# Performance work log

Hardware: AMD Instinct MI355X
Metric: run time of the kernel (lower is better)

Reference implementation:

```python
import jax, jax.numpy as jnp
import numpy as np

N = 50000
E = 800000
D = 64

def setup_inputs() -> dict:
    key = jax.random.key(0)
    k1, k2, k3, k4 = jax.random.split(key, 4)
    node_features = jax.random.normal(k1, (N, D), dtype=jnp.float32)
    edge_index = jax.random.randint(k2, (E, 2), 0, N, dtype=jnp.int64)
    W = jax.random.normal(k3, (D, D), dtype=jnp.float32) * (1.0 / np.sqrt(D))
    b_lin = jax.random.normal(k4, (D,), dtype=jnp.float32) * 0.02
    bias = jnp.zeros((D,), dtype=jnp.float32)
    return {"node_features": node_features, "edge_index": edge_index,
            "W": W, "b_lin": b_lin, "bias": bias}

def reference(node_features, edge_index, W, b_lin, bias):
    # linear: [N, D_in] @ [D_in, D_out]
    x = node_features @ W.T + b_lin
    src = edge_index[:, 0]
    dst = edge_index[:, 1]
    n = x.shape[0]
    # scatter-add of gathered source features into destination nodes
    aggregated = jax.ops.segment_sum(x[src], dst, num_segments=n)
    degree = jax.ops.segment_sum(jnp.ones((src.shape[0],), x.dtype), dst,
                                 num_segments=n)
    degree = jnp.maximum(degree, 1.0)
    x = x + aggregated / degree[:, None]
    return jax.nn.relu(x + bias)
```

## Files before the change

kernel.cpp:

```cpp
#include <hip/hip_runtime.h>
#include <hip/hip_bf16.h>

#define NN 50000
#define DD 64
#define EE 800000
#define NB 196
#define NTILE 3125
#define NSLICE 128
#define ESL 6250
#define DRNG 6250
#define BCAP 64

typedef unsigned short u16;
typedef unsigned int u32;
typedef __attribute__((ext_vector_type(8))) short bf16x8;
typedef __attribute__((ext_vector_type(4))) float f32x4;

__device__ __forceinline__ float bf2f(u16 u) {
  u32 t = ((u32)u) << 16;
  return __builtin_bit_cast(float, t);
}
__device__ __forceinline__ u16 f2bf(float f) {
  u32 b = __builtin_bit_cast(u32, f);
  u32 r = (b + 0x7FFF + ((b >> 16) & 1)) >> 16;
  return (u16)r;
}

__global__ __launch_bounds__(256) void linear_mfma_kernel(
    const float* __restrict__ nf, const float* __restrict__ W,
    const float* __restrict__ b_lin, u16* __restrict__ x16,
    int* __restrict__ cnt) {
  __shared__ u16 Wsh[64 * 72];
  int tid = threadIdx.x;

  if (blockIdx.x < NB) {
    int zi = blockIdx.x * 256 + tid;
    if (zi < NN) cnt[zi] = 0;
  }

#pragma unroll
  for (int s = 0; s < 16; ++s) {
    int idx = s * 256 + tid;
    int j = idx >> 6, k = idx & 63;
    Wsh[j * 72 + k] = f2bf(W[idx]);
  }
  __syncthreads();

  int wave = tid >> 6;
  int lane = tid & 63;
  int tile = blockIdx.x * 4 + wave;
  if (tile >= NTILE) return;

  int m = lane & 15;
  int quad = lane >> 4;
  int rowbase = tile * 16;

  bf16x8 bfrag[4][2];
#pragma unroll
  for (int c = 0; c < 4; ++c) {
#pragma unroll
    for (int ks = 0; ks < 2; ++ks) {
      const u16* p = &Wsh[(c * 16 + m) * 72 + ks * 32 + quad * 8];
      bfrag[c][ks] = *(const bf16x8*)p;
    }
  }

  bf16x8 afrag[2];
#pragma unroll
  for (int ks = 0; ks < 2; ++ks) {
    const float* p = nf + (rowbase + m) * DD + ks * 32 + quad * 8;
    float4 lo = *(const float4*)p;
    float4 hi = *(const float4*)(p + 4);
    bf16x8 a;
    a[0] = (short)f2bf(lo.x); a[1] = (short)f2bf(lo.y);
    a[2] = (short)f2bf(lo.z); a[3] = (short)f2bf(lo.w);
    a[4] = (short)f2bf(hi.x); a[5] = (short)f2bf(hi.y);
    a[6] = (short)f2bf(hi.z); a[7] = (short)f2bf(hi.w);
    afrag[ks] = a;
  }

  f32x4 acc[4];
#pragma unroll
  for (int c = 0; c < 4; ++c) {
    acc[c][0] = 0.0f; acc[c][1] = 0.0f; acc[c][2] = 0.0f; acc[c][3] = 0.0f;
  }
#pragma unroll
  for (int c = 0; c < 4; ++c) {
    acc[c] = __builtin_amdgcn_mfma_f32_16x16x32_bf16(afrag[0], bfrag[c][0], acc[c], 0, 0, 0);
    acc[c] = __builtin_amdgcn_mfma_f32_16x16x32_bf16(afrag[1], bfrag[c][1], acc[c], 0, 0, 0);
  }

#pragma unroll
  for (int c = 0; c < 4; ++c) {
    int gcol = c * 16 + m;
    float bl = b_lin[gcol];
#pragma unroll
    for (int r = 0; r < 4; ++r) {
      int grow = rowbase + quad * 4 + r;
      x16[grow * DD + gcol] = f2bf(acc[c][r] + bl);
    }
  }
}

__global__ __launch_bounds__(256) void scatter_kernel(
    const int* __restrict__ ei, int* __restrict__ cnt,
    u16* __restrict__ bucket) {
  int r = blockIdx.x & 7;
  int sl = blockIdx.x >> 3;
  int rlo = r * DRNG;
  int ebase = sl * ESL;
  int eend = ebase + ESL;
#pragma unroll 1
  for (int it = 0; it < 13; ++it) {
    int e = ebase + it * 512 + (int)threadIdx.x * 2;
    if (e < eend) {
      int4 p = *(const int4*)(ei + 2 * e);
      if ((u32)(p.y - rlo) < (u32)DRNG) {
        int pos = atomicAdd(&cnt[p.y], 1);
        if (pos < BCAP) bucket[p.y * BCAP + pos] = (u16)p.x;
      }
      if ((u32)(p.w - rlo) < (u32)DRNG) {
        int pos = atomicAdd(&cnt[p.w], 1);
        if (pos < BCAP) bucket[p.w * BCAP + pos] = (u16)p.z;
      }
    }
  }
}

template <int BASE, int LEN>
__device__ __forceinline__ float chunkN(int my, int n,
                                        const u16* __restrict__ x16, int j) {
  float v[LEN];
#pragma unroll
  for (int k = 0; k < LEN; ++k) {
    int s = __builtin_amdgcn_readlane(my, BASE + k);
    v[k] = bf2f(x16[s * DD + j]);
  }
  float a = 0.0f;
#pragma unroll
  for (int k = 0; k < LEN; ++k) a += (BASE + k < n) ? v[k] : 0.0f;
  return a;
}

__global__ __launch_bounds__(256) void gather_kernel(
    const u16* __restrict__ x16, const u16* __restrict__ bucket,
    const int* __restrict__ cnt, const float* __restrict__ bias,
    float* __restrict__ out) {
  int i = blockIdx.x * 4 + (threadIdx.x >> 6);
  int j = threadIdx.x & 63;
  int deg = cnt[i];
  int win = deg < BCAP ? deg : BCAP;
  int my = (int)bucket[i * BCAP + j];

  float acc = chunkN<0, 16>(my, win, x16, j);
  if (win > 16) acc += chunkN<16, 8>(my, win, x16, j);
  if (win > 24) acc += chunkN<24, 8>(my, win, x16, j);
  if (win > 32) acc += chunkN<32, 8>(my, win, x16, j);
  if (win > 40) acc += chunkN<40, 8>(my, win, x16, j);
  if (win > 48) acc += chunkN<48, 8>(my, win, x16, j);
  if (win > 56) acc += chunkN<56, 8>(my, win, x16, j);

  float inv = 1.0f / fmaxf((float)deg, 1.0f);
  float self = bf2f(x16[i * DD + j]);
  out[i * DD + j] = fmaxf(fmaf(acc, inv, self + bias[j]), 0.0f);
}

extern "C" void kernel_launch(void* const* d_in, const int* in_sizes, int n_in,
                              void* d_out, int out_size, void* d_ws, size_t ws_size,
                              hipStream_t stream) {
  const float* nf    = (const float*)d_in[0];
  const int*   ei    = (const int*)d_in[1];
  const float* W     = (const float*)d_in[2];
  const float* b_lin = (const float*)d_in[3];
  const float* bias  = (const float*)d_in[4];
  float* out = (float*)d_out;

  u16* x16    = (u16*)d_ws;
  u16* bucket = x16 + (size_t)NN * DD;
  int* cnt    = (int*)(bucket + (size_t)NN * BCAP);

  linear_mfma_kernel<<<(NTILE + 3) / 4, 256, 0, stream>>>(nf, W, b_lin, x16, cnt);
  scatter_kernel<<<NSLICE * 8, 256, 0, stream>>>(ei, cnt, bucket);
  gather_kernel<<<NN / 4, 256, 0, stream>>>(x16, bucket, cnt, bias, out);
}
```

Before: 135.9 us.

## Fuse linear, scatter and gather into one cooperative persistent kernel

Replaces the three separate launches with one cooperative persistent kernel of 512 blocks that uses grid-wide syncs between phases. Odd and even blocks run the linear and scatter phases in opposite order so the MFMA work and the atomic bucket filling can overlap. The aim is to remove launch gaps and per-kernel tail effects. In exchange it adds two grid barriers, limits parallelism to 512 blocks with persistent loops, and keeps the old three-kernel path as a fallback if the cooperative launch fails.

```diff
diff --git a/kernel.cpp b/kernel.cpp
--- a/kernel.cpp
+++ b/kernel.cpp
@@ -1,5 +1,7 @@
 #include <hip/hip_runtime.h>
-#include <hip/hip_bf16.h>
+#include <hip/hip_cooperative_groups.h>
+
+namespace cg = cooperative_groups;
 
 #define NN 50000
 #define DD 64
@@ -10,6 +12,8 @@
 #define ESL 6250
 #define DRNG 6250
 #define BCAP 64
+#define NVB 1024
+#define GRID 512
 
 typedef unsigned short u16;
 typedef unsigned int u32;
@@ -24,6 +28,168 @@
   u32 b = __builtin_bit_cast(u32, f);
   u32 r = (b + 0x7FFF + ((b >> 16) & 1)) >> 16;
   return (u16)r;
+}
+
+template <int STRIDE>
+__device__ __forceinline__ void do_linear(const float* __restrict__ nf,
+                                          const float* __restrict__ b_lin,
+                                          u16* __restrict__ x16,
+                                          const u16* Wsh, int tid) {
+  int wave = tid >> 6;
+  int lane = tid & 63;
+  int m = lane & 15;
+  int quad = lane >> 4;
+#pragma unroll 1
+  for (int tile = blockIdx.x * 4 + wave; tile < NTILE; tile += STRIDE * 4) {
+    int rowbase = tile * 16;
+
+    bf16x8 bfrag[4][2];
+#pragma unroll
+    for (int c = 0; c < 4; ++c) {
+#pragma unroll
+      for (int ks = 0; ks < 2; ++ks) {
+        const u16* p = &Wsh[(c * 16 + m) * 72 + ks * 32 + quad * 8];
+        bfrag[c][ks] = *(const bf16x8*)p;
+      }
+    }
+
+    bf16x8 afrag[2];
+#pragma unroll
+    for (int ks = 0; ks < 2; ++ks) {
+      const float* p = nf + (rowbase + m) * DD + ks * 32 + quad * 8;
+      float4 lo = *(const float4*)p;
+      float4 hi = *(const float4*)(p + 4);
+      bf16x8 a;
+      a[0] = (short)f2bf(lo.x); a[1] = (short)f2bf(lo.y);
+      a[2] = (short)f2bf(lo.z); a[3] = (short)f2bf(lo.w);
+      a[4] = (short)f2bf(hi.x); a[5] = (short)f2bf(hi.y);
+      a[6] = (short)f2bf(hi.z); a[7] = (short)f2bf(hi.w);
+      afrag[ks] = a;
+    }
+
+    f32x4 acc[4];
+#pragma unroll
+    for (int c = 0; c < 4; ++c) {
+      acc[c][0] = 0.0f; acc[c][1] = 0.0f; acc[c][2] = 0.0f; acc[c][3] = 0.0f;
+    }
+#pragma unroll
+    for (int c = 0; c < 4; ++c) {
+      acc[c] = __builtin_amdgcn_mfma_f32_16x16x32_bf16(afrag[0], bfrag[c][0], acc[c], 0, 0, 0);
+      acc[c] = __builtin_amdgcn_mfma_f32_16x16x32_bf16(afrag[1], bfrag[c][1], acc[c], 0, 0, 0);
+    }
+
+#pragma unroll
+    for (int c = 0; c < 4; ++c) {
+      int gcol = c * 16 + m;
+      float bl = b_lin[gcol];
+#pragma unroll
+      for (int r = 0; r < 4; ++r) {
+        int grow = rowbase + quad * 4 + r;
+        x16[grow * DD + gcol] = f2bf(acc[c][r] + bl);
+      }
+    }
+  }
+}
+
+template <int STRIDE>
+__device__ __forceinline__ void do_scatter(const int* __restrict__ ei,
+                                           int* __restrict__ cnt,
+                                           u16* __restrict__ bucket, int tid) {
+#pragma unroll 1
+  for (int vb = blockIdx.x; vb < NVB; vb += STRIDE) {
+    int r = vb & 7;
+    int sl = vb >> 3;
+    int rlo = r * DRNG;
+    int ebase = sl * ESL;
+    int eend = ebase + ESL;
+#pragma unroll 1
+    for (int it = 0; it < 13; ++it) {
+      int e = ebase + it * 512 + tid * 2;
+      if (e < eend) {
+        int4 p = *(const int4*)(ei + 2 * e);
+        if ((u32)(p.y - rlo) < (u32)DRNG) {
+          int pos = atomicAdd(&cnt[p.y], 1);
+          if (pos < BCAP) bucket[p.y * BCAP + pos] = (u16)p.x;
+        }
+        if ((u32)(p.w - rlo) < (u32)DRNG) {
+          int pos = atomicAdd(&cnt[p.w], 1);
+          if (pos < BCAP) bucket[p.w * BCAP + pos] = (u16)p.z;
+        }
+      }
+    }
+  }
+}
+
+template <int BASE, int LEN>
+__device__ __forceinline__ float chunkN(int my, int n,
+                                        const u16* __restrict__ x16, int j) {
+  float v[LEN];
+#pragma unroll
+  for (int k = 0; k < LEN; ++k) {
+    int s = __builtin_amdgcn_readlane(my, BASE + k);
+    v[k] = bf2f(x16[s * DD + j]);
+  }
+  float a = 0.0f;
+#pragma unroll
+  for (int k = 0; k < LEN; ++k) a += (BASE + k < n) ? v[k] : 0.0f;
+  return a;
+}
+
+__device__ __forceinline__ float gather_node(int i, int deg,
+                                             const u16* __restrict__ x16,
+                                             const u16* __restrict__ bucket,
+                                             int j) {
+  int win = deg < BCAP ? deg : BCAP;
+  int my = (int)bucket[i * BCAP + j];
+  float acc = chunkN<0, 16>(my, win, x16, j);
+  if (win > 16) acc += chunkN<16, 8>(my, win, x16, j);
+  if (win > 24) acc += chunkN<24, 8>(my, win, x16, j);
+  if (win > 32) acc += chunkN<32, 8>(my, win, x16, j);
+  if (win > 40) acc += chunkN<40, 8>(my, win, x16, j);
+  if (win > 48) acc += chunkN<48, 8>(my, win, x16, j);
+  if (win > 56) acc += chunkN<56, 8>(my, win, x16, j);
+  return acc;
+}
+
+__global__ __launch_bounds__(256, 2) void mega_kernel(
+    const float* __restrict__ nf, const int* __restrict__ ei,
+    const float* __restrict__ W, const float* __restrict__ b_lin,
+    const float* __restrict__ bias, u16* __restrict__ x16,
+    u16* __restrict__ bucket, int* __restrict__ cnt,
+    float* __restrict__ out) {
+  __shared__ u16 Wsh[64 * 72];
+  int tid = threadIdx.x;
+  cg::grid_group grid = cg::this_grid();
+
+#pragma unroll 1
+  for (int i = blockIdx.x * 256 + tid; i < NN; i += GRID * 256)
+    __hip_atomic_store(&cnt[i], 0, __ATOMIC_RELAXED, __HIP_MEMORY_SCOPE_AGENT);
+#pragma unroll
+  for (int s = 0; s < 16; ++s) {
+    int idx = s * 256 + tid;
+    Wsh[(idx >> 6) * 72 + (idx & 63)] = f2bf(W[idx]);
+  }
+  grid.sync();
+
+  if (blockIdx.x & 1) {
+    do_scatter<GRID>(ei, cnt, bucket, tid);
+    do_linear<GRID>(nf, b_lin, x16, Wsh, tid);
+  } else {
+    do_linear<GRID>(nf, b_lin, x16, Wsh, tid);
+    do_scatter<GRID>(ei, cnt, bucket, tid);
+  }
+  grid.sync();
+
+  int wave = tid >> 6;
+  int j = tid & 63;
+#pragma unroll 1
+  for (int i = blockIdx.x * 4 + wave; i < NN; i += GRID * 4) {
+    int deg = cnt[i];
+    float acc = gather_node(i, deg, x16, bucket, j);
+    float inv = 1.0f / fmaxf((float)deg, 1.0f);
+    float self = bf2f(x16[i * DD + j]);
+    out[i * DD + j] = fmaxf(fmaf(acc, inv, self + bias[j]), 0.0f);
+  }
 }
 
 __global__ __launch_bounds__(256) void linear_mfma_kernel(
@@ -32,72 +198,60 @@
     int* __restrict__ cnt) {
   __shared__ u16 Wsh[64 * 72];
   int tid = threadIdx.x;
-
   if (blockIdx.x < NB) {
     int zi = blockIdx.x * 256 + tid;
     if (zi < NN) cnt[zi] = 0;
   }
-
 #pragma unroll
   for (int s = 0; s < 16; ++s) {
     int idx = s * 256 + tid;
-    int j = idx >> 6, k = idx & 63;
-    Wsh[j * 72 + k] = f2bf(W[idx]);
+    Wsh[(idx >> 6) * 72 + (idx & 63)] = f2bf(W[idx]);
   }
   __syncthreads();
-
   int wave = tid >> 6;
-  int lane = tid & 63;
   int tile = blockIdx.x * 4 + wave;
   if (tile >= NTILE) return;
-
-  int m = lane & 15;
-  int quad = lane >> 4;
-  int rowbase = tile * 16;
-
-  bf16x8 bfrag[4][2];
-#pragma unroll
-  for (int c = 0; c < 4; ++c) {
+  {
+    int lane = tid & 63;
+    int m = lane & 15;
+    int quad = lane >> 4;
+    int rowbase = tile * 16;
+    bf16x8 bfrag[4][2];
+#pragma unroll
+    for (int c = 0; c < 4; ++c)
+#pragma unroll
+      for (int ks = 0; ks < 2; ++ks)
+        bfrag[c][ks] = *(const bf16x8*)&Wsh[(c * 16 + m) * 72 + ks * 32 + quad * 8];
+    bf16x8 afrag[2];
 #pragma unroll
     for (int ks = 0; ks < 2; ++ks) {
-      const u16* p = &Wsh[(c * 16 + m) * 72 + ks * 32 + quad * 8];
-      bfrag[c][ks] = *(const bf16x8*)p;
-    }
-  }
-
-  bf16x8 afrag[2];
-#pragma unroll
-  for (int ks = 0; ks < 2; ++ks) {
-    const float* p = nf + (rowbase + m) * DD + ks * 32 + quad * 8;
-    float4 lo = *(const float4*)p;
-    float4 hi = *(const float4*)(p + 4);
-    bf16x8 a;
-    a[0] = (short)f2bf(lo.x); a[1] = (short)f2bf(lo.y);
-    a[2] = (short)f2bf(lo.z); a[3] = (short)f2bf(lo.w);
-    a[4] = (short)f2bf(hi.x); a[5] = (short)f2bf(hi.y);
-    a[6] = (short)f2bf(hi.z); a[7] = (short)f2bf(hi.w);
-    afrag[ks] = a;
-  }
-
-  f32x4 acc[4];
-#pragma unroll
-  for (int c = 0; c < 4; ++c) {
-    acc[c][0] = 0.0f; acc[c][1] = 0.0f; acc[c][2] = 0.0f; acc[c][3] = 0.0f;
-  }
-#pragma unroll
-  for (int c = 0; c < 4; ++c) {
-    acc[c] = __builtin_amdgcn_mfma_f32_16x16x32_bf16(afrag[0], bfrag[c][0], acc[c], 0, 0, 0);
-    acc[c] = __builtin_amdgcn_mfma_f32_16x16x32_bf16(afrag[1], bfrag[c][1], acc[c], 0, 0, 0);
-  }
-
-#pragma unroll
-  for (int c = 0; c < 4; ++c) {
-    int gcol = c * 16 + m;
-    float bl = b_lin[gcol];
-#pragma unroll
-    for (int r = 0; r < 4; ++r) {
-      int grow = rowbase + quad * 4 + r;
-      x16[grow * DD + gcol] = f2bf(acc[c][r] + bl);
+      const float* p = nf + (rowbase + m) * DD + ks * 32 + quad * 8;
+      float4 lo = *(const float4*)p;
+      float4 hi = *(const float4*)(p + 4);
+      bf16x8 a;
+      a[0] = (short)f2bf(lo.x); a[1] = (short)f2bf(lo.y);
+      a[2] = (short)f2bf(lo.z); a[3] = (short)f2bf(lo.w);
+      a[4] = (short)f2bf(hi.x); a[5] = (short)f2bf(hi.y);
+      a[6] = (short)f2bf(hi.z); a[7] = (short)f2bf(hi.w);
+      afrag[ks] = a;
+    }
+    f32x4 acc[4];
+#pragma unroll
+    for (int c = 0; c < 4; ++c) {
+      acc[c][0] = 0.0f; acc[c][1] = 0.0f; acc[c][2] = 0.0f; acc[c][3] = 0.0f;
+    }
+#pragma unroll
+    for (int c = 0; c < 4; ++c) {
+      acc[c] = __builtin_amdgcn_mfma_f32_16x16x32_bf16(afrag[0], bfrag[c][0], acc[c], 0, 0, 0);
+      acc[c] = __builtin_amdgcn_mfma_f32_16x16x32_bf16(afrag[1], bfrag[c][1], acc[c], 0, 0, 0);
+    }
+#pragma unroll
+    for (int c = 0; c < 4; ++c) {
+      int gcol = c * 16 + m;
+      float bl = b_lin[gcol];
+#pragma unroll
+      for (int r = 0; r < 4; ++r)
+        x16[(rowbase + quad * 4 + r) * DD + gcol] = f2bf(acc[c][r] + bl);
     }
   }
 }
@@ -105,41 +259,7 @@
 __global__ __launch_bounds__(256) void scatter_kernel(
     const int* __restrict__ ei, int* __restrict__ cnt,
     u16* __restrict__ bucket) {
-  int r = blockIdx.x & 7;
-  int sl = blockIdx.x >> 3;
-  int rlo = r * DRNG;
-  int ebase = sl * ESL;
-  int eend = ebase + ESL;
-#pragma unroll 1
-  for (int it = 0; it < 13; ++it) {
-    int e = ebase + it * 512 + (int)threadIdx.x * 2;
-    if (e < eend) {
-      int4 p = *(const int4*)(ei + 2 * e);
-      if ((u32)(p.y - rlo) < (u32)DRNG) {
-        int pos = atomicAdd(&cnt[p.y], 1);
-        if (pos < BCAP) bucket[p.y * BCAP + pos] = (u16)p.x;
-      }
-      if ((u32)(p.w - rlo) < (u32)DRNG) {
-        int pos = atomicAdd(&cnt[p.w], 1);
-        if (pos < BCAP) bucket[p.w * BCAP + pos] = (u16)p.z;
-      }
-    }
-  }
-}
-
-template <int BASE, int LEN>
-__device__ __forceinline__ float chunkN(int my, int n,
-                                        const u16* __restrict__ x16, int j) {
-  float v[LEN];
-#pragma unroll
-  for (int k = 0; k < LEN; ++k) {
-    int s = __builtin_amdgcn_readlane(my, BASE + k);
-    v[k] = bf2f(x16[s * DD + j]);
-  }
-  float a = 0.0f;
-#pragma unroll
-  for (int k = 0; k < LEN; ++k) a += (BASE + k < n) ? v[k] : 0.0f;
-  return a;
+  do_scatter<NVB>(ei, cnt, bucket, (int)threadIdx.x);
 }
 
 __global__ __launch_bounds__(256) void gather_kernel(
@@ -149,17 +269,7 @@
   int i = blockIdx.x * 4 + (threadIdx.x >> 6);
   int j = threadIdx.x & 63;
   int deg = cnt[i];
-  int win = deg < BCAP ? deg : BCAP;
-  int my = (int)bucket[i * BCAP + j];
-
-  float acc = chunkN<0, 16>(my, win, x16, j);
-  if (win > 16) acc += chunkN<16, 8>(my, win, x16, j);
-  if (win > 24) acc += chunkN<24, 8>(my, win, x16, j);
-  if (win > 32) acc += chunkN<32, 8>(my, win, x16, j);
-  if (win > 40) acc += chunkN<40, 8>(my, win, x16, j);
-  if (win > 48) acc += chunkN<48, 8>(my, win, x16, j);
-  if (win > 56) acc += chunkN<56, 8>(my, win, x16, j);
-
+  float acc = gather_node(i, deg, x16, bucket, j);
   float inv = 1.0f / fmaxf((float)deg, 1.0f);
   float self = bf2f(x16[i * DD + j]);
   out[i * DD + j] = fmaxf(fmaf(acc, inv, self + bias[j]), 0.0f);
@@ -179,7 +289,14 @@
   u16* bucket = x16 + (size_t)NN * DD;
   int* cnt    = (int*)(bucket + (size_t)NN * BCAP);
 
-  linear_mfma_kernel<<<(NTILE + 3) / 4, 256, 0, stream>>>(nf, W, b_lin, x16, cnt);
-  scatter_kernel<<<NSLICE * 8, 256, 0, stream>>>(ei, cnt, bucket);
-  gather_kernel<<<NN / 4, 256, 0, stream>>>(x16, bucket, cnt, bias, out);
-}
+  void* args[] = {(void*)&nf, (void*)&ei, (void*)&W, (void*)&b_lin,
+                  (void*)&bias, (void*)&x16, (void*)&bucket, (void*)&cnt,
+                  (void*)&out};
+  hipError_t err = hipLaunchCooperativeKernel(
+      (const void*)mega_kernel, dim3(GRID), dim3(256), args, 0, stream);
+  if (err != hipSuccess) {
+    linear_mfma_kernel<<<(NTILE + 3) / 4, 256, 0, stream>>>(nf, W, b_lin, x16, cnt);
+    scatter_kernel<<<NVB, 256, 0, stream>>>(ei, cnt, bucket);
+    gather_kernel<<<NN / 4, 256, 0, stream>>>(x16, bucket, cnt, bias, out);
+  }
+}
```

Result: slower. 276.0 us (+103.0%).

## Fuse linear and scatter kernels into one launch, zero counts via memset

Applied to the files above, without the earlier changes.

Merges the MFMA linear kernel and the edge bucketing scatter kernel into a single launch whose first 1024 blocks do the scatter and the remaining blocks do the linear transform, so the two independent stages can run concurrently. Count zeroing moves from the linear kernel into a hipMemsetAsync issued beforehand, which is required because the scatter now runs alongside rather than after the zeroing. This removes a kernel boundary and lets atomic-bound scatter overlap with compute, at the cost of an extra memset call on the stream.

```diff
diff --git a/kernel.cpp b/kernel.cpp
--- a/kernel.cpp
+++ b/kernel.cpp
@@ -4,12 +4,13 @@
 #define NN 50000
 #define DD 64
 #define EE 800000
-#define NB 196
 #define NTILE 3125
 #define NSLICE 128
 #define ESL 6250
 #define DRNG 6250
 #define BCAP 64
+#define NVB 1024
+#define NLB 782
 
 typedef unsigned short u16;
 typedef unsigned int u32;
@@ -26,29 +27,48 @@
   return (u16)r;
 }
 
-__global__ __launch_bounds__(256) void linear_mfma_kernel(
-    const float* __restrict__ nf, const float* __restrict__ W,
-    const float* __restrict__ b_lin, u16* __restrict__ x16,
-    int* __restrict__ cnt) {
+__global__ __launch_bounds__(256) void fused_ls_kernel(
+    const float* __restrict__ nf, const int* __restrict__ ei,
+    const float* __restrict__ W, const float* __restrict__ b_lin,
+    u16* __restrict__ x16, u16* __restrict__ bucket, int* __restrict__ cnt) {
   __shared__ u16 Wsh[64 * 72];
+  int b = blockIdx.x;
   int tid = threadIdx.x;
 
-  if (blockIdx.x < NB) {
-    int zi = blockIdx.x * 256 + tid;
-    if (zi < NN) cnt[zi] = 0;
+  if (b < NVB) {
+    int r = b & 7;
+    int sl = b >> 3;
+    int rlo = r * DRNG;
+    int ebase = sl * ESL;
+    int eend = ebase + ESL;
+#pragma unroll 1
+    for (int it = 0; it < 13; ++it) {
+      int e = ebase + it * 512 + tid * 2;
+      if (e < eend) {
+        int4 p = *(const int4*)(ei + 2 * e);
+        if ((u32)(p.y - rlo) < (u32)DRNG) {
+          int pos = atomicAdd(&cnt[p.y], 1);
+          if (pos < BCAP) bucket[p.y * BCAP + pos] = (u16)p.x;
+        }
+        if ((u32)(p.w - rlo) < (u32)DRNG) {
+          int pos = atomicAdd(&cnt[p.w], 1);
+          if (pos < BCAP) bucket[p.w * BCAP + pos] = (u16)p.z;
+        }
+      }
+    }
+    return;
   }
 
 #pragma unroll
   for (int s = 0; s < 16; ++s) {
     int idx = s * 256 + tid;
-    int j = idx >> 6, k = idx & 63;
-    Wsh[j * 72 + k] = f2bf(W[idx]);
+    Wsh[(idx >> 6) * 72 + (idx & 63)] = f2bf(W[idx]);
   }
   __syncthreads();
 
   int wave = tid >> 6;
   int lane = tid & 63;
-  int tile = blockIdx.x * 4 + wave;
+  int tile = (b - NVB) * 4 + wave;
   if (tile >= NTILE) return;
 
   int m = lane & 15;
@@ -95,34 +115,9 @@
     int gcol = c * 16 + m;
     float bl = b_lin[gcol];
 #pragma unroll
-    for (int r = 0; r < 4; ++r) {
-      int grow = rowbase + quad * 4 + r;
-      x16[grow * DD + gcol] = f2bf(acc[c][r] + bl);
-    }
-  }
-}
-
-__global__ __launch_bounds__(256) void scatter_kernel(
-    const int* __restrict__ ei, int* __restrict__ cnt,
-    u16* __restrict__ bucket) {
-  int r = blockIdx.x & 7;
-  int sl = blockIdx.x >> 3;
-  int rlo = r * DRNG;
-  int ebase = sl * ESL;
-  int eend = ebase + ESL;
-#pragma unroll 1
-  for (int it = 0; it < 13; ++it) {
-    int e = ebase + it * 512 + (int)threadIdx.x * 2;
-    if (e < eend) {
-      int4 p = *(const int4*)(ei + 2 * e);
-      if ((u32)(p.y - rlo) < (u32)DRNG) {
-        int pos = atomicAdd(&cnt[p.y], 1);
-        if (pos < BCAP) bucket[p.y * BCAP + pos] = (u16)p.x;
-      }
-      if ((u32)(p.w - rlo) < (u32)DRNG) {
-        int pos = atomicAdd(&cnt[p.w], 1);
-        if (pos < BCAP) bucket[p.w * BCAP + pos] = (u16)p.z;
-      }
+    for (int r2 = 0; r2 < 4; ++r2) {
+      int grow = rowbase + quad * 4 + r2;
+      x16[grow * DD + gcol] = f2bf(acc[c][r2] + bl);
     }
   }
 }
@@ -179,7 +174,7 @@
   u16* bucket = x16 + (size_t)NN * DD;
   int* cnt    = (int*)(bucket + (size_t)NN * BCAP);
 
-  linear_mfma_kernel<<<(NTILE + 3) / 4, 256, 0, stream>>>(nf, W, b_lin, x16, cnt);
-  scatter_kernel<<<NSLICE * 8, 256, 0, stream>>>(ei, cnt, bucket);
+  hipMemsetAsync(cnt, 0, NN * sizeof(int), stream);
+  fused_ls_kernel<<<NVB + NLB, 256, 0, stream>>>(nf, ei, W, b_lin, x16, bucket, cnt);
   gather_kernel<<<NN / 4, 256, 0, stream>>>(x16, bucket, cnt, bias, out);
 }
```

After: 130.7 us. -3.8%, faster.
